# Kernel optimization log

Hardware: AMD Instinct MI355X
Metric: run time of the kernel (lower is better)

Reference implementation:

```python
import jax, jax.numpy as jnp
import numpy as np

NUM_TOKENS = 4096
LATENT_DIM = 256
BETA = 0.25
TEMPERATURE = 1.0  # temp_init buffer value
EPS_TEMP = 1e-6


def setup_inputs() -> dict:
    key = jax.random.key(0)
    k1, k2 = jax.random.split(key)
    latent = jax.random.normal(k1, (4, 2048, LATENT_DIM), dtype=jnp.float32)
    cb = jax.random.normal(k2, (NUM_TOKENS, LATENT_DIM), dtype=jnp.float32)
    # module normalizes codebook rows at init
    codebook = cb / jnp.linalg.norm(cb, axis=-1, keepdims=True)
    return {"latent": latent, "codebook": codebook}


def _l2norm(x):
    return x / jnp.clip(jnp.linalg.norm(x, axis=-1, keepdims=True), 1e-12)


def reference(latent, codebook):
    B, S, D = latent.shape
    flat = latent.reshape(-1, D)                       # [N, D]
    # cosine similarity via normalized matmul
    ln = _l2norm(flat)
    cn = _l2norm(codebook)
    cosine_sim = jnp.einsum('nd,kd->nk', ln, cn)       # [N, K]
    distances = 2.0 - 2.0 * cosine_sim
    scaled = distances / jnp.maximum(TEMPERATURE, EPS_TEMP)
    soft_assign = jax.nn.softmax(-scaled, axis=-1)     # [N, K]
    indices = jnp.argmax(soft_assign, axis=-1)         # [N]
    hard_assign = jax.nn.one_hot(indices, NUM_TOKENS, dtype=jnp.float32)
    # straight-through soft->hard assignment
    assign = hard_assign + soft_assign - jax.lax.stop_gradient(soft_assign)

    selected_cosine_sim = jnp.take_along_axis(cosine_sim, indices[:, None], axis=1).mean()

    # codebook pairwise euclidean diagnostics (off-diagonal mean / min)
    sq = jnp.sum(codebook * codebook, axis=-1)         # [K]
    d2 = sq[:, None] + sq[None, :] - 2.0 * (codebook @ codebook.T)
    cdist = jnp.sqrt(jnp.clip(d2, 0.0))                # [K, K]
    K = NUM_TOKENS
    off_sum = jnp.sum(cdist) - jnp.sum(jnp.diagonal(cdist))
    avg_euclidean = off_sum / (K * (K - 1))
    eye = jnp.eye(K, dtype=bool)
    min_euclidean = jnp.min(jnp.where(eye, jnp.inf, cdist))

    quantized = (assign @ codebook).reshape(B, S, D)
    commitment_loss = BETA * jnp.mean((jax.lax.stop_gradient(latent) - quantized) ** 2)
    codebook_loss = jnp.mean((latent - jax.lax.stop_gradient(quantized)) ** 2)
    quantized = latent + jax.lax.stop_gradient(quantized - latent)

    avg_probs = jnp.mean(hard_assign, axis=0)
    perplexity = jnp.exp(-jnp.sum(avg_probs * jnp.log(avg_probs + 1e-10)))

    return (quantized, indices, commitment_loss, codebook_loss, perplexity,
            selected_cosine_sim, avg_euclidean, min_euclidean)
```

## Files before the change

### kernel.cpp

```cpp
#include <hip/hip_runtime.h>
#include <hip/hip_bf16.h>
#include <math.h>

#define NTOK 8192
#define DIM 256
#define KCB 4096
#define NCB (KCB / 128)
#define NKEY 4
#define NKROW (NCB * NKEY)
#define DELTA 0.08f
#define GTIE 2e-6
#define MAXC 16
#define NSCOB2 ((NTOK / 256) * (KCB / 256))
#define NTRI2 ((KCB / 256) * (KCB / 256 + 1) / 2)
#define NPAIRB NTRI2

typedef unsigned long long ull;
typedef unsigned short ushort;
typedef __attribute__((ext_vector_type(8))) short shortx8;
typedef __attribute__((ext_vector_type(4))) float floatx4;
typedef const __attribute__((address_space(1))) void* gas_cp;
typedef __attribute__((address_space(3))) void* las_p;

__device__ __forceinline__ unsigned f2ord(float f) {
    unsigned u = __float_as_uint(f);
    return (u & 0x80000000u) ? ~u : (u | 0x80000000u);
}
__device__ __forceinline__ float ord2f(unsigned u) {
    unsigned b = (u & 0x80000000u) ? (u & 0x7FFFFFFFu) : ~u;
    return __uint_as_float(b);
}
__device__ __forceinline__ ushort f2bf(float f) {
    unsigned u = __float_as_uint(f);
    unsigned r = u + 0x7FFFu + ((u >> 16) & 1u);
    return (ushort)(r >> 16);
}

union TileSmem {
    struct { ushort a[256][64]; ushort b[256][64]; } t[2];
    unsigned keys[256][68];
    struct { float rs[512]; float rm[512]; } red;
};

__device__ __forceinline__ void stage_tile8(const ushort* __restrict__ gA,
                                            const ushort* __restrict__ gB,
                                            ushort (*la)[64], ushort (*lb)[64],
                                            int wave, int lane, int kk) {
    int p = lane & 7;
    int rsub = lane >> 3;
    int kc = p ^ rsub;
    const ushort* sa = gA + (size_t)(wave * 32 + rsub) * DIM + kk + kc * 8;
    const ushort* sb = gB + (size_t)(wave * 32 + rsub) * DIM + kk + kc * 8;
#pragma unroll
    for (int c = 0; c < 4; ++c) {
        __builtin_amdgcn_global_load_lds((gas_cp)(sa + (size_t)(c * 8) * DIM),
                                         (las_p)&la[wave * 32 + c * 8][0], 16, 0, 0);
        __builtin_amdgcn_global_load_lds((gas_cp)(sb + (size_t)(c * 8) * DIM),
                                         (las_p)&lb[wave * 32 + c * 8][0], 16, 0, 0);
    }
}
__device__ __forceinline__ shortx8 frag_read(const ushort (*lds)[64], int row,
                                             int lc) {
    return *(const shortx8*)&lds[row][(lc ^ (row & 7)) * 8];
}

__global__ __launch_bounds__(256) void prep(const float* __restrict__ lat,
                                            const float* __restrict__ cb,
                                            float* __restrict__ nrml,
                                            float* __restrict__ nrmc,
                                            ushort* __restrict__ latbf,
                                            ushort* __restrict__ cnbf,
                                            ushort* __restrict__ cbbf,
                                            float* __restrict__ sq,
                                            unsigned* __restrict__ counts) {
    int bid = blockIdx.x, t = threadIdx.x;
    int wid = t >> 6, lane = t & 63;
    int h = (lane >> 3) & 1, j = lane & 7;
    if (bid < NTOK / 4) {
        int n = bid * 4 + wid;
        if (bid < 16) counts[bid * 256 + t] = 0u;
        const float* row = lat + (size_t)n * DIM;
        int d0 = lane * 4;
        float4 xv = *(const float4*)(row + d0);
        ushort4 bv;
        bv.x = f2bf(xv.x); bv.y = f2bf(xv.y); bv.z = f2bf(xv.z); bv.w = f2bf(xv.w);
        *(ushort4*)(latbf + (size_t)n * DIM + d0) = bv;
        const float* p = row + h * 128;
        float r = __fmul_rn(p[j], p[j]);
#pragma unroll 1
        for (int i = 8; i < 128; i += 8)
            r = __fadd_rn(r, __fmul_rn(p[i + j], p[i + j]));
        float v[16];
#pragma unroll
        for (int l = 0; l < 16; ++l) v[l] = __shfl(r, l, 64);
        float h0 = __fadd_rn(__fadd_rn(__fadd_rn(v[0], v[1]), __fadd_rn(v[2], v[3])),
                             __fadd_rn(__fadd_rn(v[4], v[5]), __fadd_rn(v[6], v[7])));
        float h1 = __fadd_rn(__fadd_rn(__fadd_rn(v[8], v[9]), __fadd_rn(v[10], v[11])),
                             __fadd_rn(__fadd_rn(v[12], v[13]), __fadd_rn(v[14], v[15])));
        float nr = fmaxf(sqrtf(__fadd_rn(h0, h1)), 1e-12f);
        if (lane == 0) nrml[n] = nr;
    } else {
        int n = (bid - NTOK / 4) * 4 + wid;
        const float* row = cb + (size_t)n * DIM;
        int d0 = lane * 4;
        float4 xv = *(const float4*)(row + d0);
        const float* p = row + h * 128;
        float r = __fmul_rn(p[j], p[j]);
        double ds = 0.0;
#pragma unroll 1
        for (int i = 8; i < 128; i += 8)
            r = __fadd_rn(r, __fmul_rn(p[i + j], p[i + j]));
#pragma unroll 1
        for (int i = 0; i < 128; i += 8) { double vv = (double)p[i + j]; ds += vv * vv; }
        float v[16];
#pragma unroll
        for (int l = 0; l < 16; ++l) v[l] = __shfl(r, l, 64);
        float h0 = __fadd_rn(__fadd_rn(__fadd_rn(v[0], v[1]), __fadd_rn(v[2], v[3])),
                             __fadd_rn(__fadd_rn(v[4], v[5]), __fadd_rn(v[6], v[7])));
        float h1 = __fadd_rn(__fadd_rn(__fadd_rn(v[8], v[9]), __fadd_rn(v[10], v[11])),
                             __fadd_rn(__fadd_rn(v[12], v[13]), __fadd_rn(v[14], v[15])));
        float nr = fmaxf(sqrtf(__fadd_rn(h0, h1)), 1e-12f);
        double dsum = 0.0;
#pragma unroll 1
        for (int l = 0; l < 16; ++l) dsum += __shfl(ds, l, 64);
        if (lane == 0) { nrmc[n] = nr; sq[n] = (float)dsum; }
        ushort4 cn, cbv;
        cn.x = f2bf(xv.x / nr); cn.y = f2bf(xv.y / nr);
        cn.z = f2bf(xv.z / nr); cn.w = f2bf(xv.w / nr);
        cbv.x = f2bf(xv.x); cbv.y = f2bf(xv.y); cbv.z = f2bf(xv.z); cbv.w = f2bf(xv.w);
        *(ushort4*)(cnbf + (size_t)n * DIM + d0) = cn;
        *(ushort4*)(cbbf + (size_t)n * DIM + d0) = cbv;
    }
}

__global__ __launch_bounds__(512, 2) void gemms(const ushort* __restrict__ latbf,
                                                const ushort* __restrict__ cnbf,
                                                const ushort* __restrict__ cbbf,
                                                const float* __restrict__ sq,
                                                unsigned* __restrict__ keysw,
                                                float* __restrict__ psumw,
                                                unsigned* __restrict__ pminw) {
    __shared__ TileSmem sm;
    int tid = threadIdx.x;
    int wave = tid >> 6, lane = tid & 63;
    int quad = lane >> 4, l15 = lane & 15;
    int wr = wave >> 1, wc = wave & 1;
    bool isScore = blockIdx.x < NSCOB2;
    int rowBase, colBase, tri = 0, cbk = 0;
    const ushort *gA, *gB;
    if (isScore) {
        cbk = blockIdx.x & 15;
        int rbk = blockIdx.x >> 4;
        rowBase = rbk * 256; colBase = cbk * 256;
        gA = latbf + (size_t)rowBase * DIM;
        gB = cnbf + (size_t)colBase * DIM;
    } else {
        tri = blockIdx.x - NSCOB2;
        int a = (int)((sqrtf(8.f * tri + 1.f) - 1.f) * 0.5f);
        while ((a + 1) * (a + 2) / 2 <= tri) ++a;
        while (a * (a + 1) / 2 > tri) --a;
        int b = tri - a * (a + 1) / 2;
        rowBase = b * 256; colBase = a * 256;
        gA = cbbf + (size_t)rowBase * DIM;
        gB = cbbf + (size_t)colBase * DIM;
    }
    floatx4 acc[4][8];
#pragma unroll
    for (int m = 0; m < 4; ++m)
#pragma unroll
        for (int n = 0; n < 8; ++n) acc[m][n] = (floatx4){0.f, 0.f, 0.f, 0.f};

    stage_tile8(gA, gB, sm.t[0].a, sm.t[0].b, wave, lane, 0);
    asm volatile("s_waitcnt vmcnt(0)" ::: "memory");
    __builtin_amdgcn_s_barrier();
    asm volatile("" ::: "memory");
#pragma unroll
    for (int t = 0; t < 4; ++t) {
        int cur = t & 1;
        if (t < 3)
            stage_tile8(gA, gB, sm.t[cur ^ 1].a, sm.t[cur ^ 1].b, wave, lane,
                        (t + 1) * 64);
#pragma unroll
        for (int s = 0; s < 2; ++s) {
            shortx8 af[4], bfv[8];
#pragma unroll
            for (int mt = 0; mt < 4; ++mt)
                af[mt] = frag_read(sm.t[cur].a, wr * 64 + mt * 16 + l15, s * 4 + quad);
#pragma unroll
            for (int nt = 0; nt < 8; ++nt)
                bfv[nt] = frag_read(sm.t[cur].b, wc * 128 + nt * 16 + l15, s * 4 + quad);
#pragma unroll
            for (int mt = 0; mt < 4; ++mt)
#pragma unroll
                for (int nt = 0; nt < 8; ++nt)
                    acc[mt][nt] = __builtin_amdgcn_mfma_f32_16x16x32_bf16(
                        af[mt], bfv[nt], acc[mt][nt], 0, 0, 0);
        }
        if (t < 3) {
            asm volatile("s_waitcnt vmcnt(0)" ::: "memory");
            __builtin_amdgcn_s_barrier();
            asm volatile("" ::: "memory");
        }
    }
    __syncthreads();
    if (isScore) {
        unsigned colp2[8];
#pragma unroll
        for (int nt = 0; nt < 8; ++nt)
            colp2[nt] = 0x80000000u | (4095u - (unsigned)(colBase + wc * 128 + nt * 16 + l15));
#pragma unroll
        for (int mt = 0; mt < 4; ++mt)
#pragma unroll
            for (int reg = 0; reg < 4; ++reg) {
                unsigned b1 = 0u, b2 = 0u;
#pragma unroll
                for (int nt = 0; nt < 8; ++nt) {
                    unsigned key = (__float_as_uint(fmaxf(acc[mt][nt][reg], 0.f)) & 0x7FFFF000u)
                                   | colp2[nt];
                    unsigned lo = min(key, b1);
                    b1 = max(key, b1);
                    b2 = max(lo, b2);
                }
                int row = wr * 64 + mt * 16 + quad * 4 + reg;
                uint2 kv; kv.x = b1; kv.y = b2;
                *(uint2*)&sm.keys[row][(wc * 16 + l15) * 2] = kv;
            }
        __syncthreads();
        {
            int prow = tid >> 1, hh = tid & 1;
            unsigned a0 = 0, a1 = 0, a2 = 0, a3 = 0;
#pragma unroll
            for (int j2 = 0; j2 < 8; ++j2) {
                uint4 v4 = *(const uint4*)&sm.keys[prow][hh * 32 + j2 * 4];
                unsigned vs[4] = {v4.x, v4.y, v4.z, v4.w};
#pragma unroll
                for (int q = 0; q < 4; ++q) {
                    unsigned v = vs[q];
                    unsigned n0 = min(v, a0); a0 = max(v, a0);
                    unsigned n1 = min(n0, a1); a1 = max(n0, a1);
                    unsigned n2 = min(n1, a2); a2 = max(n1, a2);
                    a3 = max(n2, a3);
                }
            }
            size_t base = (size_t)(rowBase + prow) * NKROW + (size_t)(cbk * 2 + hh) * NKEY;
            uint4 o; o.x = a0; o.y = a1; o.z = a2; o.w = a3;
            *(uint4*)&keysw[base] = o;
        }
    } else {
        float lsum = 0.f, lmin = INFINITY;
#pragma unroll
        for (int mt = 0; mt < 4; ++mt)
#pragma unroll
            for (int reg = 0; reg < 4; ++reg) {
                int i = rowBase + wr * 64 + mt * 16 + quad * 4 + reg;
                float sqi = sq[i];
#pragma unroll
                for (int nt = 0; nt < 8; ++nt) {
                    int j2 = colBase + wc * 128 + nt * 16 + l15;
                    float d2 = sqi + sq[j2] - 2.0f * acc[mt][nt][reg];
                    float d = sqrtf(fmaxf(d2, 0.0f));
                    bool use = i < j2;
                    lsum += use ? d : 0.f;
                    lmin = fminf(lmin, use ? d : INFINITY);
                }
            }
        sm.red.rs[tid] = lsum; sm.red.rm[tid] = lmin; __syncthreads();
        for (int s = 256; s > 0; s >>= 1) {
            if (tid < s) {
                sm.red.rs[tid] += sm.red.rs[tid + s];
                sm.red.rm[tid] = fminf(sm.red.rm[tid], sm.red.rm[tid + s]);
            }
            __syncthreads();
        }
        if (tid == 0) { psumw[tri] = sm.red.rs[0]; pminw[tri] = f2ord(sm.red.rm[0]); }
    }
}

__global__ __launch_bounds__(256) void argmax_resolve(const float* __restrict__ lat,
                                                      const float* __restrict__ cb,
                                                      const float* __restrict__ nrml,
                                                      const float* __restrict__ nrmc,
                                                      const unsigned* __restrict__ keysw,
                                                      float* __restrict__ outidx,
                                                      float* __restrict__ outq,
                                                      unsigned* __restrict__ counts,
                                                      float* __restrict__ selw,
                                                      float* __restrict__ msew) {
    __shared__ int scand[4][MAXC];
    __shared__ double sc64[4][MAXC];
    int wid = threadIdx.x >> 6, lane = threadIdx.x & 63;
    int n = blockIdx.x * 4 + wid;
    const unsigned* kr = keysw + (size_t)n * NKROW;
    uint2 kv = *(const uint2*)(kr + lane * 2);
    unsigned m = max(kv.x, kv.y);
#pragma unroll
    for (int off = 1; off < 64; off <<= 1) {
        unsigned o = __shfl_xor(m, off, 64);
        m = max(m, o);
    }
    float v1 = ord2f(m & 0xFFFFF000u);
    float thresh = v1 - DELTA;
    bool p0 = ord2f(kv.x & 0xFFFFF000u) >= thresh;
    bool p1 = ord2f(kv.y & 0xFFFFF000u) >= thresh;
    ull b0 = __ballot(p0), b1 = __ballot(p1);
    int below0 = __builtin_amdgcn_mbcnt_hi((unsigned)(b0 >> 32),
                 __builtin_amdgcn_mbcnt_lo((unsigned)b0, 0));
    int below1 = __builtin_amdgcn_mbcnt_hi((unsigned)(b1 >> 32),
                 __builtin_amdgcn_mbcnt_lo((unsigned)b1, 0));
    int base1 = __popcll(b0);
    int nc = base1 + __popcll(b1);
    if (p0 && below0 < MAXC)
        scand[wid][below0] = 4095 - (int)(kv.x & 0xFFFu);
    if (p1 && base1 + below1 < MAXC)
        scand[wid][base1 + below1] = 4095 - (int)(kv.y & 0xFFFu);
    nc = nc < MAXC ? nc : MAXC;
    __threadfence_block();
    float nx = nrml[n];
    int d0 = lane * 4;
    float4 xv = *(const float4*)(lat + (size_t)n * DIM + d0);
    int idx; float selcos;
    if (nc <= 1) {
        idx = 4095 - (int)(m & 0xFFFu);
        selcos = v1 / nx;
    } else {
        float la0 = xv.x / nx, la1 = xv.y / nx, la2 = xv.z / nx, la3 = xv.w / nx;
        for (int c = 0; c < nc; ++c) {
            int k = scand[wid][c];
            float nk = nrmc[k];
            float4 cv = *(const float4*)(cb + (size_t)k * DIM + d0);
            double part = (double)(cv.x / nk) * la0 + (double)(cv.y / nk) * la1 +
                          (double)(cv.z / nk) * la2 + (double)(cv.w / nk) * la3;
#pragma unroll
            for (int off = 1; off < 64; off <<= 1) part += __shfl_xor(part, off, 64);
            if (lane == 0) sc64[wid][c] = part;
        }
        __threadfence_block();
        double best64 = -1e300;
        for (int c = 0; c < nc; ++c) best64 = fmax(best64, sc64[wid][c]);
        int nrisk = 0;
        for (int c = 0; c < nc; ++c) if (sc64[wid][c] >= best64 - GTIE) ++nrisk;
        if (nrisk == 1) {
            idx = 0x7FFFFFFF; selcos = 0.f;
            for (int c = 0; c < nc; ++c)
                if (sc64[wid][c] >= best64 - GTIE) { idx = scand[wid][c]; selcos = (float)sc64[wid][c]; }
        } else {
            ull keyf = 0ull, keym = 0ull;
            if (lane < nc && sc64[wid][lane] >= best64 - GTIE) {
                int k = scand[wid][lane];
                const float* cr = cb + (size_t)k * DIM;
                const float* x = lat + (size_t)n * DIM;
                float nk = nrmc[k];
                float af = 0.f, am = 0.f;
                for (int d = 0; d < DIM; ++d) {
                    float la = x[d] / nx;
                    float cv = cr[d] / nk;
                    af = fmaf(la, cv, af);
                    am = __fadd_rn(am, __fmul_rn(la, cv));
                }
                float df = __fsub_rn(2.0f, __fmul_rn(2.0f, af));
                float dm = __fsub_rn(2.0f, __fmul_rn(2.0f, am));
                keyf = ((ull)(0xFFFFFFFFu - f2ord(df)) << 32) | (ull)(0xFFFFFFFFu - (unsigned)k);
                keym = ((ull)(0xFFFFFFFFu - f2ord(dm)) << 32) | (ull)(0xFFFFFFFFu - (unsigned)k);
            }
#pragma unroll
            for (int off = 1; off < 64; off <<= 1) {
                ull of = __shfl_xor(keyf, off, 64);
                ull om = __shfl_xor(keym, off, 64);
                keyf = of > keyf ? of : keyf;
                keym = om > keym ? om : keym;
            }
            int colf = (int)(0xFFFFFFFFu - (unsigned)(keyf & 0xFFFFFFFFull));
            int colm = (int)(0xFFFFFFFFu - (unsigned)(keym & 0xFFFFFFFFull));
            idx = colf < colm ? colf : colm;
            selcos = 0.f;
            for (int c = 0; c < nc; ++c)
                if (scand[wid][c] == idx) selcos = (float)sc64[wid][c];
        }
    }
    float4 qv = *(const float4*)(cb + (size_t)idx * DIM + d0);
    *(float4*)(outq + (size_t)n * DIM + d0) = qv;
    float dx = xv.x - qv.x, dy = xv.y - qv.y, dz = xv.z - qv.z, dw = xv.w - qv.w;
    float msep = fmaf(dx, dx, fmaf(dy, dy, fmaf(dz, dz, dw * dw)));
#pragma unroll
    for (int off = 1; off < 64; off <<= 1) msep += __shfl_xor(msep, off, 64);
    if (lane == 0) {
        outidx[n] = (float)idx;
        atomicAdd(&counts[idx], 1u);
        selw[n] = selcos;
        msew[n] = msep;
    }
}

__global__ void finalize(const unsigned* __restrict__ counts,
                         const float* __restrict__ selw,
                         const float* __restrict__ msew,
                         const float* __restrict__ psumw,
                         const unsigned* __restrict__ pminw,
                         float* __restrict__ outs) {
    int t = threadIdx.x;
    __shared__ float red[256];
    float h = 0.f;
    for (int k = t; k < KCB; k += 256) {
        float p = (float)counts[k] * (1.0f / (float)NTOK);
        h += p * logf(p + 1e-10f);
    }
    red[t] = h; __syncthreads();
    for (int s = 128; s > 0; s >>= 1) { if (t < s) red[t] += red[t + s]; __syncthreads(); }
    float entNeg = red[0];
    __syncthreads();
    float ssel = 0.f;
    for (int k = t; k < NTOK; k += 256) ssel += selw[k];
    red[t] = ssel; __syncthreads();
    for (int s = 128; s > 0; s >>= 1) { if (t < s) red[t] += red[t + s]; __syncthreads(); }
    float selSum = red[0];
    __syncthreads();
    float sm = 0.f;
    for (int k = t; k < NTOK; k += 256) sm += msew[k];
    red[t] = sm; __syncthreads();
    for (int s = 128; s > 0; s >>= 1) { if (t < s) red[t] += red[t + s]; __syncthreads(); }
    float mseSum = red[0];
    __syncthreads();
    float ps = 0.f;
    for (int k = t; k < NPAIRB; k += 256) ps += psumw[k];
    red[t] = ps; __syncthreads();
    for (int s = 128; s > 0; s >>= 1) { if (t < s) red[t] += red[t + s]; __syncthreads(); }
    float pairSum = red[0];
    __syncthreads();
    unsigned pm = 0xFFFFFFFFu;
    for (int k = t; k < NPAIRB; k += 256) pm = min(pm, pminw[k]);
    ((unsigned*)red)[t] = pm; __syncthreads();
    for (int s = 128; s > 0; s >>= 1) {
        if (t < s) ((unsigned*)red)[t] = min(((unsigned*)red)[t], ((unsigned*)red)[t + s]);
        __syncthreads();
    }
    unsigned pairMin = ((unsigned*)red)[0];
    if (t == 0) {
        float mse = mseSum / (float)(NTOK * DIM);
        outs[0] = 0.25f * mse;
        outs[1] = mse;
        outs[2] = expf(-entNeg);
        outs[3] = selSum / (float)NTOK;
        outs[4] = pairSum * 2.0f / ((float)KCB * (float)(KCB - 1));
        outs[5] = ord2f(pairMin);
    }
}

extern "C" void kernel_launch(void* const* d_in, const int* in_sizes, int n_in,
                              void* d_out, int out_size, void* d_ws, size_t ws_size,
                              hipStream_t stream) {
    const float* latent = (const float*)d_in[0];
    const float* codebook = (const float*)d_in[1];
    float* out = (float*)d_out;
    float* outq = out;
    float* outidx = out + (size_t)NTOK * DIM;
    float* outs = outidx + NTOK;

    unsigned* keysw = (unsigned*)d_ws;
    ushort* latbf = (ushort*)(keysw + (size_t)NKROW * NTOK);
    ushort* cnbf = latbf + (size_t)NTOK * DIM;
    ushort* cbbf = cnbf + (size_t)KCB * DIM;
    float* nrml = (float*)(cbbf + (size_t)KCB * DIM);
    float* nrmc = nrml + NTOK;
    float* sq = nrmc + KCB;
    unsigned* counts = (unsigned*)(sq + KCB);
    float* selw = (float*)(counts + KCB);
    float* msew = selw + NTOK;
    float* psumw = msew + NTOK;
    unsigned* pminw = (unsigned*)(psumw + 528);

    hipLaunchKernelGGL(prep, dim3(NTOK / 4 + KCB / 4), dim3(256), 0, stream,
                       latent, codebook, nrml, nrmc, latbf, cnbf, cbbf, sq, counts);
    hipLaunchKernelGGL(gemms, dim3(NSCOB2 + NTRI2), dim3(512), 0, stream,
                       latbf, cnbf, cbbf, sq, keysw, psumw, pminw);
    hipLaunchKernelGGL(argmax_resolve, dim3(NTOK / 4), dim3(256), 0, stream,
                       latent, codebook, nrml, nrmc, keysw, outidx, outq, counts, selw, msew);
    hipLaunchKernelGGL(finalize, dim3(1), dim3(256), 0, stream, counts, selw, msew, psumw, pminw, outs);
}
```

Baseline: 167.6 us.

## Prefetch two GEMM tiles ahead, fuse finalize into resolve, unroll prep loops

The GEMM main loop now issues the first two K-tiles up front and uses a partial vmcnt wait, so the load of tile t+2 overlaps compute on tile t. It also raises wave priority around the MFMA block. The separate single-block finalize kernel is folded into argmax_resolve: a last-block-done atomic counter runs the final reductions, which removes one kernel launch. Prep loops are unrolled and the double-precision shuffle sum becomes an xor-butterfly, though its summation order may change the low bits.

```diff
diff --git a/kernel.cpp b/kernel.cpp
--- a/kernel.cpp
+++ b/kernel.cpp
@@ -72,13 +72,15 @@
                                             ushort* __restrict__ cnbf,
                                             ushort* __restrict__ cbbf,
                                             float* __restrict__ sq,
-                                            unsigned* __restrict__ counts) {
+                                            unsigned* __restrict__ counts,
+                                            unsigned* __restrict__ done) {
     int bid = blockIdx.x, t = threadIdx.x;
     int wid = t >> 6, lane = t & 63;
     int h = (lane >> 3) & 1, j = lane & 7;
     if (bid < NTOK / 4) {
         int n = bid * 4 + wid;
         if (bid < 16) counts[bid * 256 + t] = 0u;
+        if (bid == 16 && t == 0) *done = 0u;
         const float* row = lat + (size_t)n * DIM;
         int d0 = lane * 4;
         float4 xv = *(const float4*)(row + d0);
@@ -87,7 +89,7 @@
         *(ushort4*)(latbf + (size_t)n * DIM + d0) = bv;
         const float* p = row + h * 128;
         float r = __fmul_rn(p[j], p[j]);
-#pragma unroll 1
+#pragma unroll
         for (int i = 8; i < 128; i += 8)
             r = __fadd_rn(r, __fmul_rn(p[i + j], p[i + j]));
         float v[16];
@@ -107,10 +109,10 @@
         const float* p = row + h * 128;
         float r = __fmul_rn(p[j], p[j]);
         double ds = 0.0;
-#pragma unroll 1
+#pragma unroll
         for (int i = 8; i < 128; i += 8)
             r = __fadd_rn(r, __fmul_rn(p[i + j], p[i + j]));
-#pragma unroll 1
+#pragma unroll
         for (int i = 0; i < 128; i += 8) { double vv = (double)p[i + j]; ds += vv * vv; }
         float v[16];
 #pragma unroll
@@ -120,10 +122,9 @@
         float h1 = __fadd_rn(__fadd_rn(__fadd_rn(v[8], v[9]), __fadd_rn(v[10], v[11])),
                              __fadd_rn(__fadd_rn(v[12], v[13]), __fadd_rn(v[14], v[15])));
         float nr = fmaxf(sqrtf(__fadd_rn(h0, h1)), 1e-12f);
-        double dsum = 0.0;
-#pragma unroll 1
-        for (int l = 0; l < 16; ++l) dsum += __shfl(ds, l, 64);
-        if (lane == 0) { nrmc[n] = nr; sq[n] = (float)dsum; }
+#pragma unroll
+        for (int off = 1; off < 16; off <<= 1) ds += __shfl_xor(ds, off, 16);
+        if (lane == 0) { nrmc[n] = nr; sq[n] = (float)ds; }
         ushort4 cn, cbv;
         cn.x = f2bf(xv.x / nr); cn.y = f2bf(xv.y / nr);
         cn.z = f2bf(xv.z / nr); cn.w = f2bf(xv.w / nr);
@@ -171,15 +172,15 @@
         for (int n = 0; n < 8; ++n) acc[m][n] = (floatx4){0.f, 0.f, 0.f, 0.f};
 
     stage_tile8(gA, gB, sm.t[0].a, sm.t[0].b, wave, lane, 0);
-    asm volatile("s_waitcnt vmcnt(0)" ::: "memory");
-    __builtin_amdgcn_s_barrier();
-    asm volatile("" ::: "memory");
+    stage_tile8(gA, gB, sm.t[1].a, sm.t[1].b, wave, lane, 64);
 #pragma unroll
     for (int t = 0; t < 4; ++t) {
         int cur = t & 1;
         if (t < 3)
-            stage_tile8(gA, gB, sm.t[cur ^ 1].a, sm.t[cur ^ 1].b, wave, lane,
-                        (t + 1) * 64);
+            asm volatile("s_waitcnt vmcnt(8)" ::: "memory");
+        else
+            asm volatile("s_waitcnt vmcnt(0)" ::: "memory");
+        __builtin_amdgcn_s_barrier();
 #pragma unroll
         for (int s = 0; s < 2; ++s) {
             shortx8 af[4], bfv[8];
@@ -189,18 +190,18 @@
 #pragma unroll
             for (int nt = 0; nt < 8; ++nt)
                 bfv[nt] = frag_read(sm.t[cur].b, wc * 128 + nt * 16 + l15, s * 4 + quad);
+            __builtin_amdgcn_s_setprio(1);
 #pragma unroll
             for (int mt = 0; mt < 4; ++mt)
 #pragma unroll
                 for (int nt = 0; nt < 8; ++nt)
                     acc[mt][nt] = __builtin_amdgcn_mfma_f32_16x16x32_bf16(
                         af[mt], bfv[nt], acc[mt][nt], 0, 0, 0);
-        }
-        if (t < 3) {
-            asm volatile("s_waitcnt vmcnt(0)" ::: "memory");
-            __builtin_amdgcn_s_barrier();
-            asm volatile("" ::: "memory");
-        }
+            __builtin_amdgcn_s_setprio(0);
+        }
+        __builtin_amdgcn_s_barrier();
+        if (t < 2)
+            stage_tile8(gA, gB, sm.t[cur].a, sm.t[cur].b, wave, lane, (t + 2) * 64);
     }
     __syncthreads();
     if (isScore) {
@@ -285,7 +286,11 @@
                                                       float* __restrict__ outq,
                                                       unsigned* __restrict__ counts,
                                                       float* __restrict__ selw,
-                                                      float* __restrict__ msew) {
+                                                      float* __restrict__ msew,
+                                                      const float* __restrict__ psumw,
+                                                      const unsigned* __restrict__ pminw,
+                                                      unsigned* __restrict__ done,
+                                                      float* __restrict__ outs) {
     __shared__ int scand[4][MAXC];
     __shared__ double sc64[4][MAXC];
     int wid = threadIdx.x >> 6, lane = threadIdx.x & 63;
@@ -389,59 +394,65 @@
         selw[n] = selcos;
         msew[n] = msep;
     }
-}
-
-__global__ void finalize(const unsigned* __restrict__ counts,
-                         const float* __restrict__ selw,
-                         const float* __restrict__ msew,
-                         const float* __restrict__ psumw,
-                         const unsigned* __restrict__ pminw,
-                         float* __restrict__ outs) {
-    int t = threadIdx.x;
-    __shared__ float red[256];
-    float h = 0.f;
-    for (int k = t; k < KCB; k += 256) {
-        float p = (float)counts[k] * (1.0f / (float)NTOK);
-        h += p * logf(p + 1e-10f);
-    }
-    red[t] = h; __syncthreads();
-    for (int s = 128; s > 0; s >>= 1) { if (t < s) red[t] += red[t + s]; __syncthreads(); }
-    float entNeg = red[0];
+    __shared__ unsigned isLast;
+    __threadfence();
+    if (threadIdx.x == 0)
+        isLast = (atomicAdd(done, 1u) == (unsigned)gridDim.x - 1u) ? 1u : 0u;
     __syncthreads();
-    float ssel = 0.f;
-    for (int k = t; k < NTOK; k += 256) ssel += selw[k];
-    red[t] = ssel; __syncthreads();
-    for (int s = 128; s > 0; s >>= 1) { if (t < s) red[t] += red[t + s]; __syncthreads(); }
-    float selSum = red[0];
-    __syncthreads();
-    float sm = 0.f;
-    for (int k = t; k < NTOK; k += 256) sm += msew[k];
-    red[t] = sm; __syncthreads();
-    for (int s = 128; s > 0; s >>= 1) { if (t < s) red[t] += red[t + s]; __syncthreads(); }
-    float mseSum = red[0];
-    __syncthreads();
-    float ps = 0.f;
-    for (int k = t; k < NPAIRB; k += 256) ps += psumw[k];
-    red[t] = ps; __syncthreads();
-    for (int s = 128; s > 0; s >>= 1) { if (t < s) red[t] += red[t + s]; __syncthreads(); }
-    float pairSum = red[0];
-    __syncthreads();
-    unsigned pm = 0xFFFFFFFFu;
-    for (int k = t; k < NPAIRB; k += 256) pm = min(pm, pminw[k]);
-    ((unsigned*)red)[t] = pm; __syncthreads();
-    for (int s = 128; s > 0; s >>= 1) {
-        if (t < s) ((unsigned*)red)[t] = min(((unsigned*)red)[t], ((unsigned*)red)[t + s]);
+    if (!isLast) return;
+    __threadfence();
+    {
+        int t = threadIdx.x;
+        __shared__ float red[256];
+        float hsum = 0.f;
+        for (int k = t; k < KCB; k += 256) {
+            unsigned c = __hip_atomic_load(&counts[k], __ATOMIC_RELAXED,
+                                           __HIP_MEMORY_SCOPE_AGENT);
+            float p = (float)c * (1.0f / (float)NTOK);
+            hsum += p * logf(p + 1e-10f);
+        }
+        red[t] = hsum; __syncthreads();
+        for (int s = 128; s > 0; s >>= 1) { if (t < s) red[t] += red[t + s]; __syncthreads(); }
+        float entNeg = red[0];
         __syncthreads();
-    }
-    unsigned pairMin = ((unsigned*)red)[0];
-    if (t == 0) {
-        float mse = mseSum / (float)(NTOK * DIM);
-        outs[0] = 0.25f * mse;
-        outs[1] = mse;
-        outs[2] = expf(-entNeg);
-        outs[3] = selSum / (float)NTOK;
-        outs[4] = pairSum * 2.0f / ((float)KCB * (float)(KCB - 1));
-        outs[5] = ord2f(pairMin);
+        float ssel = 0.f;
+        for (int k = t; k < NTOK; k += 256)
+            ssel += __hip_atomic_load(&selw[k], __ATOMIC_RELAXED, __HIP_MEMORY_SCOPE_AGENT);
+        red[t] = ssel; __syncthreads();
+        for (int s = 128; s > 0; s >>= 1) { if (t < s) red[t] += red[t + s]; __syncthreads(); }
+        float selSum = red[0];
+        __syncthreads();
+        float smm = 0.f;
+        for (int k = t; k < NTOK; k += 256)
+            smm += __hip_atomic_load(&msew[k], __ATOMIC_RELAXED, __HIP_MEMORY_SCOPE_AGENT);
+        red[t] = smm; __syncthreads();
+        for (int s = 128; s > 0; s >>= 1) { if (t < s) red[t] += red[t + s]; __syncthreads(); }
+        float mseSum = red[0];
+        __syncthreads();
+        float ps = 0.f;
+        for (int k = t; k < NPAIRB; k += 256) ps += psumw[k];
+        red[t] = ps; __syncthreads();
+        for (int s = 128; s > 0; s >>= 1) { if (t < s) red[t] += red[t + s]; __syncthreads(); }
+        float pairSum = red[0];
+        __syncthreads();
+        unsigned pm = 0xFFFFFFFFu;
+        for (int k = t; k < NPAIRB; k += 256) pm = min(pm, pminw[k]);
+        ((unsigned*)red)[t] = pm; __syncthreads();
+        for (int s = 128; s > 0; s >>= 1) {
+            if (t < s) ((unsigned*)red)[t] = min(((unsigned*)red)[t], ((unsigned*)red)[t + s]);
+            __syncthreads();
+        }
+        unsigned pairMin = ((unsigned*)red)[0];
+        if (t == 0) {
+            float mse = mseSum / (float)(NTOK * DIM);
+            float* outs2 = outs;
+            outs2[0] = 0.25f * mse;
+            outs2[1] = mse;
+            outs2[2] = expf(-entNeg);
+            outs2[3] = selSum / (float)NTOK;
+            outs2[4] = pairSum * 2.0f / ((float)KCB * (float)(KCB - 1));
+            outs2[5] = ord2f(pairMin);
+        }
     }
 }
 
@@ -467,12 +478,13 @@
     float* msew = selw + NTOK;
     float* psumw = msew + NTOK;
     unsigned* pminw = (unsigned*)(psumw + 528);
+    unsigned* done = pminw + 528;
 
     hipLaunchKernelGGL(prep, dim3(NTOK / 4 + KCB / 4), dim3(256), 0, stream,
-                       latent, codebook, nrml, nrmc, latbf, cnbf, cbbf, sq, counts);
+                       latent, codebook, nrml, nrmc, latbf, cnbf, cbbf, sq, counts, done);
     hipLaunchKernelGGL(gemms, dim3(NSCOB2 + NTRI2), dim3(512), 0, stream,
                        latbf, cnbf, cbbf, sq, keysw, psumw, pminw);
     hipLaunchKernelGGL(argmax_resolve, dim3(NTOK / 4), dim3(256), 0, stream,
-                       latent, codebook, nrml, nrmc, keysw, outidx, outq, counts, selw, msew);
-    hipLaunchKernelGGL(finalize, dim3(1), dim3(256), 0, stream, counts, selw, msew, psumw, pminw, outs);
-}
+                       latent, codebook, nrml, nrmc, keysw, outidx, outq, counts,
+                       selw, msew, psumw, pminw, done, outs);
+}
```

Result: slower. 324.7 us (+93.8%).
